# Kernel optimization log

Hardware: AMD Instinct MI355X
Metric: run time of the kernel (lower is better)

The kernel has to match this reference:

```python
import jax, jax.numpy as jnp
import numpy as np
from jax import lax

FEAT_STRIDE = 16
RATIOS = np.array([0.5, 1.0, 2.0], np.float32)
SCALES = np.array([8.0, 16.0, 32.0], np.float32)
A = RATIOS.size * SCALES.size            # 9 anchors per location
N_PRE = 3000                             # pre-NMS top-k (TEST-style config)
N_POST = 300                             # post-NMS rois per image
NMS_THRESH = 0.7
MIN_SIZE = 16.0
B, C, HF, WF = 4, 512, 50, 50


def setup_inputs() -> dict:
    key = jax.random.key(0)
    ks = jax.random.split(key, 4)
    mid = 512
    return {
        "inputs": jax.random.normal(ks[0], (B, C, HF, WF), jnp.float32),
        "conv_w": jax.random.normal(ks[1], (mid, C, 3, 3), jnp.float32) * 0.01,
        "conv_b": jnp.zeros((mid,), jnp.float32),
        "bf_w": jax.random.normal(ks[2], (A * 2, mid, 1, 1), jnp.float32) * 0.01,
        "bf_b": jnp.zeros((A * 2,), jnp.float32),
        "loc_w": jax.random.normal(ks[3], (A * 4, mid, 1, 1), jnp.float32) * 0.01,
        "loc_b": jnp.zeros((A * 4,), jnp.float32),
        "img_h": 800,
        "img_w": 800,
    }


def _conv(x, w, b, pad):
    y = lax.conv_general_dilated(x, w, (1, 1), [(pad, pad), (pad, pad)],
                                 dimension_numbers=("NCHW", "OIHW", "NCHW"))
    return y + b[None, :, None, None]


def _anchors(hf, wf):
    ratios = jnp.asarray(RATIOS)
    scales = jnp.asarray(SCALES)
    hs = (FEAT_STRIDE * scales[None, :] * jnp.sqrt(ratios[:, None])).reshape(-1)
    ws = (FEAT_STRIDE * scales[None, :] * jnp.sqrt(1.0 / ratios[:, None])).reshape(-1)
    c = FEAT_STRIDE / 2.0
    base = jnp.stack([c - hs / 2, c - ws / 2, c + hs / 2, c + ws / 2], 1)  # [A,4] yxyx
    sy = jnp.arange(hf, dtype=jnp.float32) * FEAT_STRIDE
    sx = jnp.arange(wf, dtype=jnp.float32) * FEAT_STRIDE
    yy, xx = jnp.meshgrid(sy, sx, indexing="ij")
    shifts = jnp.stack([yy, xx, yy, xx], -1).reshape(-1, 1, 4)
    return (shifts + base[None]).reshape(-1, 4)  # [hf*wf*A, 4]


def _decode(anchors, loc):
    # anchors [N,4] yxyx, loc [B,N,4] (dy,dx,dh,dw)
    ah = anchors[:, 2] - anchors[:, 0]
    aw = anchors[:, 3] - anchors[:, 1]
    acy = anchors[:, 0] + 0.5 * ah
    acx = anchors[:, 1] + 0.5 * aw
    cy = loc[..., 0] * ah + acy
    cx = loc[..., 1] * aw + acx
    h = jnp.exp(loc[..., 2]) * ah
    w = jnp.exp(loc[..., 3]) * aw
    return jnp.stack([cy - 0.5 * h, cx - 0.5 * w, cy + 0.5 * h, cx + 0.5 * w], -1)


def _nms(boxes, scores):
    # boxes [N,4], scores [N] -> fixed-size [N_POST,4] rois (zero-padded)
    hs = boxes[:, 2] - boxes[:, 0]
    ws = boxes[:, 3] - boxes[:, 1]
    valid = (hs >= MIN_SIZE) & (ws >= MIN_SIZE)
    s = jnp.where(valid, scores, -jnp.inf)
    order = jnp.argsort(-s)[:N_PRE]
    b = boxes[order]
    v = valid[order]
    sb = lax.stop_gradient(b)
    area = (sb[:, 2] - sb[:, 0]) * (sb[:, 3] - sb[:, 1])
    tl = jnp.maximum(sb[:, None, :2], sb[None, :, :2])
    br = jnp.minimum(sb[:, None, 2:], sb[None, :, 2:])
    wh = jnp.clip(br - tl, 0.0)
    inter = wh[..., 0] * wh[..., 1]
    iou = inter / (area[:, None] + area[None, :] - inter + 1e-9)

    def body(i, keep):
        sup = jnp.any((iou[i] > NMS_THRESH) & keep)
        return keep.at[i].set(v[i] & ~sup)

    keep = lax.fori_loop(0, N_PRE, body, jnp.zeros((N_PRE,), bool))
    pos = jnp.where(keep, jnp.cumsum(keep) - 1, N_POST)  # invalid -> dropped
    return jnp.zeros((N_POST, 4), boxes.dtype).at[pos].set(b, mode="drop")


def reference(inputs, conv_w, conv_b, bf_w, bf_b, loc_w, loc_b, img_h, img_w):
    b_, _, hf, wf = inputs.shape
    feat = jax.nn.relu(_conv(inputs, conv_w, conv_b, 1))
    loc = _conv(feat, loc_w, loc_b, 0).transpose(0, 2, 3, 1).reshape(b_, -1, 4)
    logits = _conv(feat, bf_w, bf_b, 0).transpose(0, 2, 3, 1).reshape(b_, hf, wf, A, 2)
    probs = jax.nn.softmax(logits, axis=4)
    fg = probs[..., 1].reshape(b_, -1)             # foreground scores [B, hf*wf*A]
    bf_pred = probs.reshape(b_, -1, 2)
    anchors = _anchors(hf, wf)
    boxes = _decode(anchors, loc)
    boxes = jnp.stack([
        jnp.clip(boxes[..., 0], 0.0, img_h), jnp.clip(boxes[..., 1], 0.0, img_w),
        jnp.clip(boxes[..., 2], 0.0, img_h), jnp.clip(boxes[..., 3], 0.0, img_w)], -1)
    rois = jax.vmap(_nms)(boxes, fg).reshape(-1, 4)         # [B*N_POST, 4]
    rois_idx = jnp.repeat(jnp.arange(b_, dtype=jnp.int32), N_POST)
    return rois, rois_idx, anchors, loc, bf_pred
```

## Files before the change

kernel.cpp:

```cpp
#include <hip/hip_runtime.h>
#include <hip/hip_bf16.h>
#include <math.h>

#define BIMG   4
#define CIN    512
#define MID    512
#define HF     50
#define WF     50
#define PIX    2500
#define MTOT   10000
#define ANC    9
#define NLOC   22500
#define NPRE   3000
#define NPOST  300
#define WORDS  47
#define ROWPAD 3008
#define WSTRIDE 48
#define CAP    8192

#define ROIS_OFF 0
#define IDX_OFF  4800
#define ANC_OFF  6000
#define LOC_OFF  96000
#define BF_OFF   456000

#define WS_WT     0UL
#define WS_W1T    9437184UL
#define WS_FEAT   9568256UL
#define WS_SCORE  30048256UL
#define WS_BOXD   30768256UL
#define WS_SBD    33648256UL
#define WS_M      34032256UL
#define WS_CAND   38652544UL
#define WS_CNT    38783616UL
#define WS_PART1  38786048UL
#define WS_NEED_SPLIT (WS_PART1 + 20480000UL)

__global__ __launch_bounds__(256) void prep_kernel(
    const float* __restrict__ conv_w, const float* __restrict__ loc_w,
    const float* __restrict__ bf_w, float* __restrict__ Wt, float* __restrict__ W1t) {
  int o = blockIdx.x * 256 + threadIdx.x;
  if (o < 4608 * 512) {
    int co  = o & 511;
    int k   = o >> 9;
    int c   = k & 511;
    int tap = k >> 9;
    Wt[o] = conv_w[(co * 512 + c) * 9 + tap];
  } else {
    int o2 = o - 4608 * 512;
    if (o2 < 512 * 64) {
      int co = o2 & 63;
      int c  = o2 >> 6;
      float v = 0.0f;
      if (co < 36)      v = loc_w[co * 512 + c];
      else if (co < 54) v = bf_w[(co - 36) * 512 + c];
      W1t[o2] = v;
    }
  }
}

__device__ __forceinline__ void stage_load(
    int kb, int sg, bool in0, bool in1,
    int y0, int x0, int y1, int x1,
    const float* __restrict__ ib0, const float* __restrict__ ib1, float av[8]) {
  int tap = kb >> 5;
  int c0  = (kb & 31) << 4;
  int t3  = tap / 3;
  int dy  = t3 - 1;
  int dx  = tap - t3 * 3 - 1;
  int iy0 = y0 + dy, ix0 = x0 + dx;
  int iy1 = y1 + dy, ix1 = x1 + dx;
  bool ok0 = in0 && ((unsigned)iy0 < (unsigned)HF) && ((unsigned)ix0 < (unsigned)WF);
  bool ok1 = in1 && ((unsigned)iy1 < (unsigned)HF) && ((unsigned)ix1 < (unsigned)WF);
  int base = (c0 + sg * 4) * PIX;
  int o0 = iy0 * WF + ix0;
  int o1 = iy1 * WF + ix1;
#pragma unroll
  for (int j = 0; j < 4; ++j) {
    av[2 * j]     = ok0 ? ib0[base + j * PIX + o0] : 0.0f;
    av[2 * j + 1] = ok1 ? ib1[base + j * PIX + o1] : 0.0f;
  }
}

__global__ __launch_bounds__(256, 3) void conv3x3_kernel(
    const float* __restrict__ in, const float* __restrict__ Wt,
    float* __restrict__ part0, float* __restrict__ part1) {
  __shared__ float As[2][16][128];
  const int tid = threadIdx.x;
  const int q0 = blockIdx.x * 128;
  const int lane = tid & 63;
  const int wv = tid >> 6;
  const int col0 = __builtin_amdgcn_readfirstlane(blockIdx.y * 64 + wv * 16);
  const int half = 288 / gridDim.z;
  const int kb0 = blockIdx.z * half;
  float* __restrict__ dst = (blockIdx.z == 0) ? part0 : part1;

  const int sg = tid >> 6;
  const int sp = tid & 63;
  int qs0 = q0 + 2 * sp, qs1 = qs0 + 1;
  bool in0 = qs0 < MTOT, in1 = qs1 < MTOT;
  int t0 = in0 ? qs0 : 0, t1 = in1 ? qs1 : 0;
  int b0i = t0 / PIX, r0 = t0 - b0i * PIX, y0 = r0 / WF, x0 = r0 - y0 * WF;
  int b1i = t1 / PIX, r1 = t1 - b1i * PIX, y1 = r1 / WF, x1 = r1 - y1 * WF;
  const float* ib0 = in + (size_t)b0i * (CIN * PIX);
  const float* ib1 = in + (size_t)b1i * (CIN * PIX);

  double acc[2][16];
  float accf[2][16];
#pragma unroll
  for (int p = 0; p < 2; ++p)
#pragma unroll
    for (int c = 0; c < 16; ++c) { acc[p][c] = 0.0; accf[p][c] = 0.0f; }

  {
    float av[8];
    stage_load(kb0, sg, in0, in1, y0, x0, y1, x1, ib0, ib1, av);
#pragma unroll
    for (int j = 0; j < 4; ++j)
      *(float2*)&As[0][sg * 4 + j][2 * sp] = make_float2(av[2 * j], av[2 * j + 1]);
  }
  __syncthreads();

  for (int kbl = 0; kbl < half; ++kbl) {
    int kb = kb0 + kbl;
    int cur = kbl & 1;
    float av[8];
    bool has_next = (kbl + 1 < half);
    if (has_next)
      stage_load(kb + 1, sg, in0, in1, y0, x0, y1, x1, ib0, ib1, av);

    const float* __restrict__ Bw = Wt + (size_t)(kb * 16) * 512 + col0;
#pragma unroll
    for (int kg = 0; kg < 4; ++kg) {
#pragma unroll
      for (int kq = 0; kq < 4; ++kq) {
        int kk = kg * 4 + kq;
        const float* __restrict__ br = Bw + (size_t)kk * 512;
        float2 a = *(const float2*)&As[cur][kk][2 * lane];
#pragma unroll
        for (int c = 0; c < 16; ++c) {
          float bv = br[c];
          accf[0][c] = fmaf(a.x, bv, accf[0][c]);
          accf[1][c] = fmaf(a.y, bv, accf[1][c]);
        }
      }
    }
    if (kbl & 1) {
#pragma unroll
      for (int p = 0; p < 2; ++p)
#pragma unroll
        for (int c = 0; c < 16; ++c) {
          acc[p][c] += (double)accf[p][c];
          accf[p][c] = 0.0f;
        }
    }
    if (has_next) {
      int nxt = cur ^ 1;
#pragma unroll
      for (int j = 0; j < 4; ++j)
        *(float2*)&As[nxt][sg * 4 + j][2 * sp] = make_float2(av[2 * j], av[2 * j + 1]);
    }
    __syncthreads();
  }

#pragma unroll
  for (int p = 0; p < 2; ++p) {
    int q = q0 + 2 * lane + p;
    if (q < MTOT) {
      float o[16];
#pragma unroll
      for (int c = 0; c < 16; ++c) o[c] = (float)acc[p][c];
      float* fp = &dst[(size_t)q * 512 + col0];
#pragma unroll
      for (int g = 0; g < 4; ++g)
        *(float4*)&fp[g * 4] = make_float4(o[g*4], o[g*4+1], o[g*4+2], o[g*4+3]);
    }
  }
}

__global__ __launch_bounds__(256) void combine_kernel(
    const float* __restrict__ p0, const float* __restrict__ p1,
    const float* __restrict__ bias, float* __restrict__ feat, int nz) {
  int i = blockIdx.x * 256 + threadIdx.x;
  if (i >= MTOT * 128) return;
  int c0 = (i & 127) << 2;
  float4 a = ((const float4*)p0)[i];
  float4 bs = *(const float4*)&bias[c0];
  double sx = (double)a.x, sy = (double)a.y, sz = (double)a.z, sw = (double)a.w;
  if (nz > 1) {
    float4 b = ((const float4*)p1)[i];
    sx += (double)b.x; sy += (double)b.y; sz += (double)b.z; sw += (double)b.w;
  }
  float4 o;
  o.x = (float)fmax(sx + (double)bs.x, 0.0);
  o.y = (float)fmax(sy + (double)bs.y, 0.0);
  o.z = (float)fmax(sz + (double)bs.z, 0.0);
  o.w = (float)fmax(sw + (double)bs.w, 0.0);
  ((float4*)feat)[i] = o;
}

__global__ __launch_bounds__(256) void conv1x1_kernel(
    const float* __restrict__ feat, const float* __restrict__ W1t,
    const float* __restrict__ locb, const float* __restrict__ bfb,
    double* __restrict__ rawd) {
  __shared__ float As[16][128];
  const int tid = threadIdx.x;
  const int q0 = blockIdx.x * 128;
  const int lane = tid & 63;
  const int wv = tid >> 6;
  const int col0 = __builtin_amdgcn_readfirstlane(wv * 16);

  const int pixL = tid >> 1;
  const int ch   = (tid & 1) * 8;
  const int qL   = q0 + pixL;
  const bool okL = qL < MTOT;

  double acc[2][16];
  float accf[2][16];
#pragma unroll
  for (int p = 0; p < 2; ++p)
#pragma unroll
    for (int c = 0; c < 16; ++c) { acc[p][c] = 0.0; accf[p][c] = 0.0f; }

  for (int kb = 0; kb < 32; ++kb) {
    int c0 = kb * 16;
    float4 f0 = make_float4(0, 0, 0, 0), f1 = make_float4(0, 0, 0, 0);
    if (okL) {
      const float* fp = &feat[(size_t)qL * 512 + c0 + ch];
      f0 = *(const float4*)fp;
      f1 = *(const float4*)(fp + 4);
    }
    __syncthreads();
    As[ch + 0][pixL] = f0.x; As[ch + 1][pixL] = f0.y;
    As[ch + 2][pixL] = f0.z; As[ch + 3][pixL] = f0.w;
    As[ch + 4][pixL] = f1.x; As[ch + 5][pixL] = f1.y;
    As[ch + 6][pixL] = f1.z; As[ch + 7][pixL] = f1.w;
    __syncthreads();

    const float* __restrict__ Bw = W1t + (size_t)c0 * 64 + col0;
#pragma unroll
    for (int kk = 0; kk < 16; ++kk) {
      const float* __restrict__ br = Bw + (size_t)kk * 64;
      float2 a = *(const float2*)&As[kk][2 * lane];
#pragma unroll
      for (int c = 0; c < 16; ++c) {
        float bv = br[c];
        accf[0][c] = fmaf(a.x, bv, accf[0][c]);
        accf[1][c] = fmaf(a.y, bv, accf[1][c]);
      }
    }
    if (kb & 1) {
#pragma unroll
      for (int p = 0; p < 2; ++p)
#pragma unroll
        for (int c = 0; c < 16; ++c) {
          acc[p][c] += (double)accf[p][c];
          accf[p][c] = 0.0f;
        }
    }
  }

  double bs[16];
#pragma unroll
  for (int c = 0; c < 16; ++c) {
    int co = col0 + c;
    bs[c] = (co < 36) ? (double)locb[co] : ((co < 54) ? (double)bfb[co - 36] : 0.0);
  }
#pragma unroll
  for (int p = 0; p < 2; ++p) {
    int q = q0 + 2 * lane + p;
    if (q < MTOT) {
      double* rp = &rawd[(size_t)q * 64 + col0];
#pragma unroll
      for (int c = 0; c < 16; ++c) rp[c] = acc[p][c] + bs[c];
    }
  }
}

__global__ __launch_bounds__(256) void epilogue_kernel(
    const double* __restrict__ rawd, float* __restrict__ d_out,
    double* __restrict__ boxd, unsigned long long* __restrict__ ukey,
    const int* __restrict__ imh, const int* __restrict__ imw) {
  int idx = blockIdx.x * 256 + threadIdx.x;
  if (idx >= BIMG * NLOC) return;
  int b = idx / NLOC;
  int i = idx - b * NLOC;
  int p = i / ANC;
  int a = i - p * ANC;
  int y = p / WF;
  int x = p - y * WF;
  int q = b * PIX + p;

  double l0d = rawd[(size_t)q * 64 + a * 4 + 0];
  double l1d = rawd[(size_t)q * 64 + a * 4 + 1];
  double l2d = rawd[(size_t)q * 64 + a * 4 + 2];
  double l3d = rawd[(size_t)q * 64 + a * 4 + 3];
  float4 lo = make_float4((float)l0d, (float)l1d, (float)l2d, (float)l3d);
  *(float4*)&d_out[LOC_OFF + (size_t)idx * 4] = lo;

  double g0 = rawd[(size_t)q * 64 + 36 + a * 2];
  double g1 = rawd[(size_t)q * 64 + 37 + a * 2];
  double m  = fmax(g0, g1);
  double e0 = exp(g0 - m), e1 = exp(g1 - m);
  double s  = e0 + e1;
  double p0 = e0 / s, p1 = e1 / s;
  *(float2*)&d_out[BF_OFF + (size_t)idx * 2] = make_float2((float)p0, (float)p1);

  int ridx = a / 3, sidx = a - ridx * 3;
  double ratio = (ridx == 0) ? 0.5 : ((ridx == 1) ? 1.0 : 2.0);
  double scale = (sidx == 0) ? 8.0 : ((sidx == 1) ? 16.0 : 32.0);
  double hs = 16.0 * scale * sqrt(ratio);
  double ws = 16.0 * scale * sqrt(1.0 / ratio);
  double sy = (double)(y * 16), sx = (double)(x * 16);
  double a0 = sy + (8.0 - hs * 0.5);
  double a1 = sx + (8.0 - ws * 0.5);
  double a2 = sy + (8.0 + hs * 0.5);
  double a3 = sx + (8.0 + ws * 0.5);
  if (b == 0) {
    *(float4*)&d_out[ANC_OFF + (size_t)i * 4] =
        make_float4((float)a0, (float)a1, (float)a2, (float)a3);
  }

  double ah = a2 - a0, aw = a3 - a1;
  double acy = a0 + 0.5 * ah, acx = a1 + 0.5 * aw;
  double cy = l0d * ah + acy;
  double cx = l1d * aw + acx;
  double hh = exp(l2d) * ah;
  double ww = exp(l3d) * aw;
  double ihf = (double)imh[0], iwf = (double)imw[0];
  double b0 = fmin(fmax(cy - 0.5 * hh, 0.0), ihf);
  double b1 = fmin(fmax(cx - 0.5 * ww, 0.0), iwf);
  double b2 = fmin(fmax(cy + 0.5 * hh, 0.0), ihf);
  double b3 = fmin(fmax(cx + 0.5 * ww, 0.0), iwf);
  double* bp = &boxd[(size_t)idx * 4];
  bp[0] = b0; bp[1] = b1; bp[2] = b2; bp[3] = b3;

  bool valid = (b2 - b0 >= 16.0) && (b3 - b1 >= 16.0);
  double d = valid ? (g1 - g0) : -INFINITY;
  long long bits = __double_as_longlong(d);
  unsigned long long u = (bits < 0)
      ? ~(unsigned long long)bits
      : ((unsigned long long)bits | 0x8000000000000000ull);
  ukey[idx] = ~u;
}

__global__ __launch_bounds__(1024) void thresh_kernel(
    const unsigned long long* __restrict__ ukey,
    unsigned* __restrict__ ccnt, unsigned* __restrict__ cand) {
  __shared__ unsigned hist[16384];
  __shared__ unsigned csum[1024];
  __shared__ unsigned sT, scnt;
  int b = blockIdx.x;
  int tid = threadIdx.x;
  for (int i = tid; i < 16384; i += 1024) hist[i] = 0;
  if (tid == 0) scnt = 0;
  __syncthreads();
  for (int j = tid; j < NLOC; j += 1024)
    atomicAdd(&hist[(unsigned)(ukey[(size_t)b * NLOC + j] >> 50)], 1u);
  __syncthreads();
  unsigned s = 0;
#pragma unroll
  for (int k = 0; k < 16; ++k) s += hist[tid * 16 + k];
  csum[tid] = s;
  __syncthreads();
  if (tid == 0) {
    unsigned cum = 0;
    int T = 16383;
    for (int c = 0; c < 1024; ++c) {
      if (cum + csum[c] >= NPRE) {
        unsigned cc = cum;
        for (int k = 0; k < 16; ++k) {
          cc += hist[c * 16 + k];
          if (cc >= NPRE) { T = c * 16 + k; break; }
        }
        break;
      }
      cum += csum[c];
    }
    sT = (unsigned)T;
  }
  __syncthreads();
  unsigned T = sT;
  for (int j = tid; j < NLOC; j += 1024) {
    if ((unsigned)(ukey[(size_t)b * NLOC + j] >> 50) <= T) {
      unsigned slot = atomicAdd(&scnt, 1u);
      if (slot < CAP) cand[(size_t)b * CAP + slot] = (unsigned)j;
    }
  }
  __syncthreads();
  if (tid == 0) ccnt[b] = scnt;
}

__global__ __launch_bounds__(256) void rank_kernel(
    const unsigned long long* __restrict__ ukey, const unsigned* __restrict__ ccnt,
    const unsigned* __restrict__ cand, const double* __restrict__ boxd,
    double* __restrict__ sbd) {
  __shared__ unsigned long long kt[256];
  __shared__ unsigned it[256];
  int b = blockIdx.y;
  int C = (int)min(ccnt[b], (unsigned)CAP);
  int s = blockIdx.x * 256 + threadIdx.x;
  bool act = s < C;
  unsigned myi = act ? cand[(size_t)b * CAP + s] : 0xFFFFFFFFu;
  unsigned long long ki = act ? ukey[(size_t)b * NLOC + myi] : ~0ull;
  int cnt = 0;
  int ntile = (C + 255) >> 8;
  for (int t = 0; t < ntile; ++t) {
    int j = t * 256 + threadIdx.x;
    unsigned ji = (j < C) ? cand[(size_t)b * CAP + j] : 0xFFFFFFFFu;
    kt[threadIdx.x] = (j < C) ? ukey[(size_t)b * NLOC + ji] : ~0ull;
    it[threadIdx.x] = ji;
    __syncthreads();
#pragma unroll 8
    for (int jj = 0; jj < 256; ++jj) {
      unsigned long long kj = kt[jj];
      unsigned jidx = it[jj];
      cnt += ((kj < ki) || (kj == ki && jidx < myi)) ? 1 : 0;
    }
    __syncthreads();
  }
  if (act && cnt < NPRE) {
    const double* bx = &boxd[((size_t)b * NLOC + myi) * 4];
    double* dp = &sbd[((size_t)b * NPRE + cnt) * 4];
    dp[0] = bx[0]; dp[1] = bx[1]; dp[2] = bx[2]; dp[3] = bx[3];
  }
}

__global__ __launch_bounds__(64) void nmsmask_kernel(
    const double* __restrict__ sbd, unsigned long long* __restrict__ M) {
  __shared__ double cb[64][4];
  int b = blockIdx.z;
  int jw = blockIdx.y;
  int i  = blockIdx.x * 64 + threadIdx.x;
  int j  = jw * 64 + threadIdx.x;
  double j0 = 0, j1 = 0, j2 = 0, j3 = 0;
  if (j < NPRE) {
    const double* bp = &sbd[((size_t)b * NPRE + j) * 4];
    j0 = bp[0]; j1 = bp[1]; j2 = bp[2]; j3 = bp[3];
  }
  cb[threadIdx.x][0] = j0; cb[threadIdx.x][1] = j1;
  cb[threadIdx.x][2] = j2; cb[threadIdx.x][3] = j3;
  __syncthreads();
  if (i >= NPRE) return;
  const double* bp = &sbd[((size_t)b * NPRE + i) * 4];
  double i0 = bp[0], i1 = bp[1], i2 = bp[2], i3 = bp[3];
  double ai = (i2 - i0) * (i3 - i1);
  unsigned long long mask = 0ull;
#pragma unroll 4
  for (int t = 0; t < 64; ++t) {
    double aj = (cb[t][2] - cb[t][0]) * (cb[t][3] - cb[t][1]);
    double h = fmax(fmin(i2, cb[t][2]) - fmax(i0, cb[t][0]), 0.0);
    double w = fmax(fmin(i3, cb[t][3]) - fmax(i1, cb[t][1]), 0.0);
    double inter = h * w;
    double iou = inter / (ai + aj - inter + 1e-9);
    mask |= ((iou > 0.7) ? 1ull : 0ull) << t;
  }
  M[((size_t)b * ROWPAD + i) * WSTRIDE + jw] = mask;
}

__global__ __launch_bounds__(64) void nms_scan_kernel(
    const double* __restrict__ sbd, const unsigned long long* __restrict__ M,
    float* __restrict__ d_out) {
  int b = blockIdx.x;
  int lane = threadIdx.x;
  for (int k = lane; k < NPOST; k += 64) {
    *(float4*)&d_out[ROIS_OFF + (size_t)(b * NPOST + k) * 4] = make_float4(0, 0, 0, 0);
    d_out[IDX_OFF + b * NPOST + k] = (float)b;
  }
  __syncthreads();

  unsigned long long R = ~0ull;
  if (lane < WORDS) R = 0ull;
  for (int w = 0; w < WORDS; ++w) {
    int j = w * 64 + lane;
    bool inval = true;
    if (j < NPRE) {
      const double* bp = &sbd[((size_t)b * NPRE + j) * 4];
      double h = bp[2] - bp[0], wd = bp[3] - bp[1];
      inval = !(h >= 16.0 && wd >= 16.0);
    }
    unsigned long long bal = __ballot(inval ? 1 : 0);
    if (lane == w) R |= bal;
  }

  int kept = 0;
  while (kept < NPOST) {
    unsigned long long hz = __ballot(((~R) != 0ull) ? 1 : 0);
    if (hz == 0ull) break;
    int w0 = __ffsll(hz) - 1;
    unsigned long long word = __shfl(R, w0);
    int bit = __ffsll(~word) - 1;
    int i = w0 * 64 + bit;
    if (lane < 4)
      d_out[ROIS_OFF + (size_t)(b * NPOST + kept) * 4 + lane] =
          (float)sbd[((size_t)b * NPRE + i) * 4 + lane];
    kept++;
    if (kept >= NPOST) break;
    unsigned long long row = (lane < WORDS)
        ? M[((size_t)b * ROWPAD + i) * WSTRIDE + lane] : 0ull;
    R |= row;
    if (lane == w0) R |= (1ull << bit);
  }
}

extern "C" void kernel_launch(void* const* d_in, const int* in_sizes, int n_in,
                              void* d_out, int out_size, void* d_ws, size_t ws_size,
                              hipStream_t stream) {
  const float* in     = (const float*)d_in[0];
  const float* conv_w = (const float*)d_in[1];
  const float* conv_b = (const float*)d_in[2];
  const float* bf_w   = (const float*)d_in[3];
  const float* bf_b   = (const float*)d_in[4];
  const float* loc_w  = (const float*)d_in[5];
  const float* loc_b  = (const float*)d_in[6];
  const int*   imh    = (const int*)d_in[7];
  const int*   imw    = (const int*)d_in[8];
  float* out = (float*)d_out;

  char* ws = (char*)d_ws;
  float*  Wt    = (float*)(ws + WS_WT);
  double* rawd  = (double*)(ws + WS_WT);
  float*  W1t   = (float*)(ws + WS_W1T);
  float*  feat  = (float*)(ws + WS_FEAT);
  unsigned long long* ukey = (unsigned long long*)(ws + WS_SCORE);
  double* boxd  = (double*)(ws + WS_BOXD);
  double* sbd   = (double*)(ws + WS_SBD);
  unsigned long long* M = (unsigned long long*)(ws + WS_M);
  unsigned* cand = (unsigned*)(ws + WS_CAND);
  unsigned* ccnt = (unsigned*)(ws + WS_CNT);
  float*  part1 = (float*)(ws + WS_PART1);

  const int nz = (ws_size >= WS_NEED_SPLIT) ? 2 : 1;

  hipLaunchKernelGGL(prep_kernel, dim3((4608 * 512 + 512 * 64 + 255) / 256), dim3(256),
                     0, stream, conv_w, loc_w, bf_w, Wt, W1t);
  hipLaunchKernelGGL(conv3x3_kernel, dim3(79, 8, nz), dim3(256), 0, stream,
                     in, Wt, feat, part1);
  hipLaunchKernelGGL(combine_kernel, dim3((MTOT * 128 + 255) / 256), dim3(256), 0, stream,
                     feat, part1, conv_b, feat, nz);
  hipLaunchKernelGGL(conv1x1_kernel, dim3(79), dim3(256), 0, stream,
                     feat, W1t, loc_b, bf_b, rawd);
  hipLaunchKernelGGL(epilogue_kernel, dim3((BIMG * NLOC + 255) / 256), dim3(256), 0, stream,
                     rawd, out, boxd, ukey, imh, imw);
  hipLaunchKernelGGL(thresh_kernel, dim3(4), dim3(1024), 0, stream, ukey, ccnt, cand);
  hipLaunchKernelGGL(rank_kernel, dim3(CAP / 256, 4), dim3(256), 0, stream,
                     ukey, ccnt, cand, boxd, sbd);
  hipLaunchKernelGGL(nmsmask_kernel, dim3(47, 47, 4), dim3(64), 0, stream, sbd, M);
  hipLaunchKernelGGL(nms_scan_kernel, dim3(4), dim3(64), 0, stream, sbd, M, out);
}
```

Baseline: 1.402 ms.

## Split conv3x3 K over four partials and fold combine into conv1x1 load

New measurement: 1.387 ms. Within noise of the previous version (-1.0%).

```diff
diff --git a/kernel.cpp b/kernel.cpp
--- a/kernel.cpp
+++ b/kernel.cpp
@@ -34,7 +34,10 @@
 #define WS_CAND   38652544UL
 #define WS_CNT    38783616UL
 #define WS_PART1  38786048UL
-#define WS_NEED_SPLIT (WS_PART1 + 20480000UL)
+#define WS_PART2  59266048UL
+#define WS_PART3  79746048UL
+#define WS_NEED2  59266048UL
+#define WS_NEED4  100226048UL
 
 __global__ __launch_bounds__(256) void prep_kernel(
     const float* __restrict__ conv_w, const float* __restrict__ loc_w,
@@ -84,7 +87,8 @@
 
 __global__ __launch_bounds__(256, 3) void conv3x3_kernel(
     const float* __restrict__ in, const float* __restrict__ Wt,
-    float* __restrict__ part0, float* __restrict__ part1) {
+    float* __restrict__ part0, float* __restrict__ part1,
+    float* __restrict__ part2, float* __restrict__ part3) {
   __shared__ float As[2][16][128];
   const int tid = threadIdx.x;
   const int q0 = blockIdx.x * 128;
@@ -93,7 +97,9 @@
   const int col0 = __builtin_amdgcn_readfirstlane(blockIdx.y * 64 + wv * 16);
   const int half = 288 / gridDim.z;
   const int kb0 = blockIdx.z * half;
-  float* __restrict__ dst = (blockIdx.z == 0) ? part0 : part1;
+  float* __restrict__ dst = (blockIdx.z == 0) ? part0 :
+                            (blockIdx.z == 1) ? part1 :
+                            (blockIdx.z == 2) ? part2 : part3;
 
   const int sg = tid >> 6;
   const int sp = tid & 63;
@@ -178,29 +184,10 @@
   }
 }
 
-__global__ __launch_bounds__(256) void combine_kernel(
+__global__ __launch_bounds__(256) void conv1x1_kernel(
     const float* __restrict__ p0, const float* __restrict__ p1,
-    const float* __restrict__ bias, float* __restrict__ feat, int nz) {
-  int i = blockIdx.x * 256 + threadIdx.x;
-  if (i >= MTOT * 128) return;
-  int c0 = (i & 127) << 2;
-  float4 a = ((const float4*)p0)[i];
-  float4 bs = *(const float4*)&bias[c0];
-  double sx = (double)a.x, sy = (double)a.y, sz = (double)a.z, sw = (double)a.w;
-  if (nz > 1) {
-    float4 b = ((const float4*)p1)[i];
-    sx += (double)b.x; sy += (double)b.y; sz += (double)b.z; sw += (double)b.w;
-  }
-  float4 o;
-  o.x = (float)fmax(sx + (double)bs.x, 0.0);
-  o.y = (float)fmax(sy + (double)bs.y, 0.0);
-  o.z = (float)fmax(sz + (double)bs.z, 0.0);
-  o.w = (float)fmax(sw + (double)bs.w, 0.0);
-  ((float4*)feat)[i] = o;
-}
-
-__global__ __launch_bounds__(256) void conv1x1_kernel(
-    const float* __restrict__ feat, const float* __restrict__ W1t,
+    const float* __restrict__ p2, const float* __restrict__ p3, int nz,
+    const float* __restrict__ convb, const float* __restrict__ W1t,
     const float* __restrict__ locb, const float* __restrict__ bfb,
     double* __restrict__ rawd) {
   __shared__ float As[16][128];
@@ -224,17 +211,46 @@
 
   for (int kb = 0; kb < 32; ++kb) {
     int c0 = kb * 16;
-    float4 f0 = make_float4(0, 0, 0, 0), f1 = make_float4(0, 0, 0, 0);
+    float fv[8];
+#pragma unroll
+    for (int k = 0; k < 8; ++k) fv[k] = 0.0f;
     if (okL) {
-      const float* fp = &feat[(size_t)qL * 512 + c0 + ch];
-      f0 = *(const float4*)fp;
-      f1 = *(const float4*)(fp + 4);
+      const size_t base = (size_t)qL * 512 + c0 + ch;
+      double s[8];
+      float4 a0 = *(const float4*)&p0[base];
+      float4 a1 = *(const float4*)&p0[base + 4];
+      s[0] = (double)a0.x; s[1] = (double)a0.y; s[2] = (double)a0.z; s[3] = (double)a0.w;
+      s[4] = (double)a1.x; s[5] = (double)a1.y; s[6] = (double)a1.z; s[7] = (double)a1.w;
+      if (nz > 1) {
+        float4 b0 = *(const float4*)&p1[base];
+        float4 b1 = *(const float4*)&p1[base + 4];
+        s[0] += (double)b0.x; s[1] += (double)b0.y; s[2] += (double)b0.z; s[3] += (double)b0.w;
+        s[4] += (double)b1.x; s[5] += (double)b1.y; s[6] += (double)b1.z; s[7] += (double)b1.w;
+      }
+      if (nz > 2) {
+        float4 c0v = *(const float4*)&p2[base];
+        float4 c1v = *(const float4*)&p2[base + 4];
+        s[0] += (double)c0v.x; s[1] += (double)c0v.y; s[2] += (double)c0v.z; s[3] += (double)c0v.w;
+        s[4] += (double)c1v.x; s[5] += (double)c1v.y; s[6] += (double)c1v.z; s[7] += (double)c1v.w;
+        float4 d0 = *(const float4*)&p3[base];
+        float4 d1 = *(const float4*)&p3[base + 4];
+        s[0] += (double)d0.x; s[1] += (double)d0.y; s[2] += (double)d0.z; s[3] += (double)d0.w;
+        s[4] += (double)d1.x; s[5] += (double)d1.y; s[6] += (double)d1.z; s[7] += (double)d1.w;
+      }
+      float4 bs0 = *(const float4*)&convb[c0 + ch];
+      float4 bs1 = *(const float4*)&convb[c0 + ch + 4];
+      fv[0] = (float)fmax(s[0] + (double)bs0.x, 0.0);
+      fv[1] = (float)fmax(s[1] + (double)bs0.y, 0.0);
+      fv[2] = (float)fmax(s[2] + (double)bs0.z, 0.0);
+      fv[3] = (float)fmax(s[3] + (double)bs0.w, 0.0);
+      fv[4] = (float)fmax(s[4] + (double)bs1.x, 0.0);
+      fv[5] = (float)fmax(s[5] + (double)bs1.y, 0.0);
+      fv[6] = (float)fmax(s[6] + (double)bs1.z, 0.0);
+      fv[7] = (float)fmax(s[7] + (double)bs1.w, 0.0);
     }
     __syncthreads();
-    As[ch + 0][pixL] = f0.x; As[ch + 1][pixL] = f0.y;
-    As[ch + 2][pixL] = f0.z; As[ch + 3][pixL] = f0.w;
-    As[ch + 4][pixL] = f1.x; As[ch + 5][pixL] = f1.y;
-    As[ch + 6][pixL] = f1.z; As[ch + 7][pixL] = f1.w;
+#pragma unroll
+    for (int k = 0; k < 8; ++k) As[ch + k][pixL] = fv[k];
     __syncthreads();
 
     const float* __restrict__ Bw = W1t + (size_t)c0 * 64 + col0;
@@ -521,7 +537,7 @@
   float*  Wt    = (float*)(ws + WS_WT);
   double* rawd  = (double*)(ws + WS_WT);
   float*  W1t   = (float*)(ws + WS_W1T);
-  float*  feat  = (float*)(ws + WS_FEAT);
+  float*  part0 = (float*)(ws + WS_FEAT);
   unsigned long long* ukey = (unsigned long long*)(ws + WS_SCORE);
   double* boxd  = (double*)(ws + WS_BOXD);
   double* sbd   = (double*)(ws + WS_SBD);
@@ -529,17 +545,17 @@
   unsigned* cand = (unsigned*)(ws + WS_CAND);
   unsigned* ccnt = (unsigned*)(ws + WS_CNT);
   float*  part1 = (float*)(ws + WS_PART1);
-
-  const int nz = (ws_size >= WS_NEED_SPLIT) ? 2 : 1;
+  float*  part2 = (float*)(ws + WS_PART2);
+  float*  part3 = (float*)(ws + WS_PART3);
+
+  const int nz = (ws_size >= WS_NEED4) ? 4 : ((ws_size >= WS_NEED2) ? 2 : 1);
 
   hipLaunchKernelGGL(prep_kernel, dim3((4608 * 512 + 512 * 64 + 255) / 256), dim3(256),
                      0, stream, conv_w, loc_w, bf_w, Wt, W1t);
   hipLaunchKernelGGL(conv3x3_kernel, dim3(79, 8, nz), dim3(256), 0, stream,
-                     in, Wt, feat, part1);
-  hipLaunchKernelGGL(combine_kernel, dim3((MTOT * 128 + 255) / 256), dim3(256), 0, stream,
-                     feat, part1, conv_b, feat, nz);
+                     in, Wt, part0, part1, part2, part3);
   hipLaunchKernelGGL(conv1x1_kernel, dim3(79), dim3(256), 0, stream,
-                     feat, W1t, loc_b, bf_b, rawd);
+                     part0, part1, part2, part3, nz, conv_b, W1t, loc_b, bf_b, rawd);
   hipLaunchKernelGGL(epilogue_kernel, dim3((BIMG * NLOC + 255) / 256), dim3(256), 0, stream,
                      rawd, out, boxd, ukey, imh, imw);
   hipLaunchKernelGGL(thresh_kernel, dim3(4), dim3(1024), 0, stream, ukey, ccnt, cand);
```
